# Kernel tuning notes

Measured on AMD Instinct MI355X. Metric: run time of the kernel, lower is better.

The kernel has to match this reference:

```python
import jax, jax.numpy as jnp
import numpy as np

B, S, D, H, HD = 1, 4096, 768, 12, 64
L, C, WIN, NCLS = 2, 256, 256, 64
NC = S // C
V, FF = 50265, 3072
NEG = -1e9
SCALE = np.float32(1.0 / np.sqrt(HD))


def setup_inputs() -> dict:
    key = jax.random.key(0)
    ks = jax.random.split(key, 32)
    p = lambda k, shape: (0.02 * jax.random.normal(k, shape)).astype(jnp.float32)
    inp = {
        'x': jax.random.randint(ks[0], (B, S), 0, V, dtype=jnp.int32),
        'mask_src': jnp.ones((B, S), dtype=jnp.int32),
        'clss': jnp.sort(jax.random.randint(ks[1], (B, NCLS), 0, S, dtype=jnp.int32), axis=-1),
        'segs': jax.random.randint(ks[2], (B, S), 0, 2, dtype=jnp.int32),
        'word_emb': p(ks[3], (V, D)),
        'pos_emb': p(ks[4], (S, D)),
        'type_emb': p(ks[5], (2, D)),
        'ln_e_s': jnp.ones((D,), jnp.float32), 'ln_e_b': jnp.zeros((D,), jnp.float32),
        'Wq': p(ks[6], (L, D, D)), 'bq': jnp.zeros((L, D), jnp.float32),
        'Wk': p(ks[7], (L, D, D)), 'bk': jnp.zeros((L, D), jnp.float32),
        'Wv': p(ks[8], (L, D, D)), 'bv': jnp.zeros((L, D), jnp.float32),
        'Wqg': p(ks[9], (L, D, D)), 'bqg': jnp.zeros((L, D), jnp.float32),
        'Wkg': p(ks[10], (L, D, D)), 'bkg': jnp.zeros((L, D), jnp.float32),
        'Wvg': p(ks[11], (L, D, D)), 'bvg': jnp.zeros((L, D), jnp.float32),
        'Wo': p(ks[12], (L, D, D)), 'bo': jnp.zeros((L, D), jnp.float32),
        'ln1_s': jnp.ones((L, D), jnp.float32), 'ln1_b': jnp.zeros((L, D), jnp.float32),
        'Wf1': p(ks[13], (L, D, FF)), 'bf1': jnp.zeros((L, FF), jnp.float32),
        'Wf2': p(ks[14], (L, FF, D)), 'bf2': jnp.zeros((L, D), jnp.float32),
        'ln2_s': jnp.ones((L, D), jnp.float32), 'ln2_b': jnp.zeros((L, D), jnp.float32),
    }
    return inp


def _layer_norm(x, s, b):
    m = jnp.mean(x, -1, keepdims=True)
    v = jnp.mean((x - m) ** 2, -1, keepdims=True)
    return (x - m) * jax.lax.rsqrt(v + 1e-5) * s + b


def _forward(x, mask_src, clss, segs, word_emb, pos_emb, type_emb, ln_e_s, ln_e_b,
             Wq, bq, Wk, bk, Wv, bv, Wqg, bqg, Wkg, bkg, Wvg, bvg, Wo, bo,
             ln1_s, ln1_b, Wf1, bf1, Wf2, bf2, ln2_s, ln2_b):
    # global positions: union of all clss values, same for every batch row
    g_idx = clss.reshape(-1)                                       # [NCLS]
    is_glb = jnp.zeros((S,), bool).at[g_idx].set(True)             # [S]
    kvalid = (mask_src > 0) & (~is_glb)[None, :]                   # band keys: no pad, no global
    gi = (jnp.arange(NC) * C)[:, None] + jnp.arange(3 * C)[None, :]  # gather idx into padded seq
    rel = jnp.arange(3 * C)[None, :] - (jnp.arange(C)[:, None] + C)  # key offset from query
    band_ok = jnp.abs(rel) <= WIN                                   # [C,3C]
    kv3 = jnp.pad(kvalid, ((0, 0), (C, C)))[:, gi]                  # [B,NC,3C]
    bmask = band_ok[None, None, None, :, :] & kv3[:, None, :, None, :]  # [B,1,NC,C,3C]
    gkey_ok = (mask_src[:, g_idx] > 0)[:, None, None, :]            # [B,1,1,NCLS]
    full_ok = (mask_src > 0)[:, None, None, :]                      # [B,1,1,S]

    h = _layer_norm(word_emb[x] + pos_emb[jnp.arange(S)][None] + type_emb[segs], ln_e_s, ln_e_b)

    for l in range(L):
        q = ((h @ Wq[l] + bq[l]).reshape(B, S, H, HD)) * SCALE
        k = (h @ Wk[l] + bk[l]).reshape(B, S, H, HD)
        v = (h @ Wv[l] + bv[l]).reshape(B, S, H, HD)
        # --- sliding-window band attention ---
        k3 = jnp.pad(k, ((0, 0), (C, C), (0, 0), (0, 0)))[:, gi]    # [B,NC,3C,H,HD]
        v3 = jnp.pad(v, ((0, 0), (C, C), (0, 0), (0, 0)))[:, gi]
        qc = q.reshape(B, NC, C, H, HD)
        sb = jnp.einsum('bnqhd,bnkhd->bhnqk', qc, k3)               # [B,H,NC,C,3C]
        sb = jnp.where(bmask, sb, NEG)
        # --- global keys seen by every query ---
        kg, vg = k[:, g_idx], v[:, g_idx]                           # [B,NCLS,H,HD]
        sg = jnp.einsum('bshd,bkhd->bhsk', q, kg)                   # [B,H,S,NCLS]
        sg = jnp.where(gkey_ok, sg, NEG)
        scores = jnp.concatenate([sg, sb.reshape(B, H, S, 3 * C)], -1)
        probs = jax.nn.softmax(scores, axis=-1)
        pg = probs[..., :NCLS]
        pb = probs[..., NCLS:].reshape(B, H, NC, C, 3 * C)
        out = jnp.einsum('bhnqk,bnkhd->bnqhd', pb, v3).reshape(B, S, H, HD)
        out = out + jnp.einsum('bhsk,bkhd->bshd', pg, vg)
        # --- global query tokens: full attention with *_global projections ---
        hg = h[:, g_idx]                                            # [B,NCLS,D]
        qg = ((hg @ Wqg[l] + bqg[l]).reshape(B, NCLS, H, HD)) * SCALE
        kgf = (h @ Wkg[l] + bkg[l]).reshape(B, S, H, HD)
        vgf = (h @ Wvg[l] + bvg[l]).reshape(B, S, H, HD)
        sfull = jnp.einsum('bqhd,bkhd->bhqk', qg, kgf)              # [B,H,NCLS,S]
        sfull = jnp.where(full_ok, sfull, NEG)
        og = jnp.einsum('bhqk,bkhd->bqhd', jax.nn.softmax(sfull, -1), vgf)
        out = out.at[:, g_idx].set(og)
        # --- output proj, residual, LN, FFN ---
        attn_out = out.reshape(B, S, D) @ Wo[l] + bo[l]
        h = _layer_norm(h + attn_out, ln1_s[l], ln1_b[l])
        ff = jax.nn.gelu(h @ Wf1[l] + bf1[l]) @ Wf2[l] + bf2[l]
        h = _layer_norm(h + ff, ln2_s[l], ln2_b[l])
    return h


def reference(x, mask_src, clss, segs, word_emb, pos_emb, type_emb, ln_e_s, ln_e_b,
              Wq, bq, Wk, bk, Wv, bv, Wqg, bqg, Wkg, bkg, Wvg, bvg, Wo, bo,
              ln1_s, ln1_b, Wf1, bf1, Wf2, bf2, ln2_s, ln2_b):
    return _forward(x, mask_src, clss, segs, word_emb, pos_emb, type_emb, ln_e_s, ln_e_b,
                    Wq, bq, Wk, bk, Wv, bv, Wqg, bqg, Wkg, bkg, Wvg, bvg, Wo, bo,
                    ln1_s, ln1_b, Wf1, bf1, Wf2, bf2, ln2_s, ln2_b)
```

## Files before the change

### kernel.cpp

```cpp
#include <hip/hip_runtime.h>
#include <hip/hip_bf16.h>
#include <cstdint>

#define SEQ  4096
#define DIM  768
#define NH   12
#define HDIM 64
#define NLAYER 2
#define CHK  256
#define WINR 256
#define NCLS 64
#define NCHK 16
#define FFD  3072
#define QSCALE 0.125f
#define LOG2E 1.44269504f
#define QSC2 (QSCALE * LOG2E)
#define SD ((size_t)SEQ * DIM)
#define PS_LD 72
#define TK 64
#define DEFER_THR 8.0f

typedef __attribute__((__vector_size__(16))) float floatx4;
typedef __attribute__((ext_vector_type(8))) __bf16 bf16x8;
typedef __attribute__((ext_vector_type(4))) __bf16 bf16x4;

__device__ __forceinline__ void async16(const void* g, void* l) {
    __builtin_amdgcn_global_load_lds(
        (const __attribute__((address_space(1))) uint32_t*)g,
        (__attribute__((address_space(3))) uint32_t*)l, 16, 0, 0);
}

__device__ __forceinline__ float gelu_f(float x) {
    float x3 = x * x * x;
    return 0.5f * x * (1.0f + tanhf(0.7978845608028654f * (x + 0.044715f * x3)));
}

__global__ __launch_bounds__(256) void embed_ln_kernel(
    const int* __restrict__ x, const int* __restrict__ segs,
    const float* __restrict__ word_emb, const float* __restrict__ pos_emb,
    const float* __restrict__ type_emb, const float* __restrict__ gs,
    const float* __restrict__ gb, float* __restrict__ h, __bf16* __restrict__ hb,
    int* __restrict__ isglb)
{
    int wave = threadIdx.x >> 6, lane = threadIdx.x & 63;
    int s = blockIdx.x * 4 + wave;
    if (lane == 0) isglb[s] = 0;
    int w = x[s], sg = segs[s];
    const float4* wp = (const float4*)(word_emb + (size_t)w * DIM);
    const float4* pp = (const float4*)(pos_emb + (size_t)s * DIM);
    const float4* tp = (const float4*)(type_emb + (size_t)sg * DIM);
    float4 v[3]; float lsum = 0.f;
    #pragma unroll
    for (int i = 0; i < 3; i++) {
        int d4 = lane + i * 64;
        float4 a = wp[d4], b = pp[d4], c = tp[d4];
        float4 r;
        r.x = a.x + b.x + c.x; r.y = a.y + b.y + c.y;
        r.z = a.z + b.z + c.z; r.w = a.w + b.w + c.w;
        v[i] = r; lsum += r.x + r.y + r.z + r.w;
    }
    #pragma unroll
    for (int st = 32; st > 0; st >>= 1) lsum += __shfl_xor(lsum, st);
    float mean = lsum * (1.0f / DIM);
    float lv = 0.f;
    #pragma unroll
    for (int i = 0; i < 3; i++) {
        float dx = v[i].x - mean, dy = v[i].y - mean, dz = v[i].z - mean, dw = v[i].w - mean;
        lv += dx * dx + dy * dy + dz * dz + dw * dw;
    }
    #pragma unroll
    for (int st = 32; st > 0; st >>= 1) lv += __shfl_xor(lv, st);
    float rstd = rsqrtf(lv * (1.0f / DIM) + 1e-5f);
    #pragma unroll
    for (int i = 0; i < 3; i++) {
        int d4 = lane + i * 64;
        float4 s4v = ((const float4*)gs)[d4], b4v = ((const float4*)gb)[d4];
        float4 o;
        o.x = (v[i].x - mean) * rstd * s4v.x + b4v.x;
        o.y = (v[i].y - mean) * rstd * s4v.y + b4v.y;
        o.z = (v[i].z - mean) * rstd * s4v.z + b4v.z;
        o.w = (v[i].w - mean) * rstd * s4v.w + b4v.w;
        ((float4*)(h + (size_t)s * DIM))[d4] = o;
        bf16x4 ob; ob[0] = (__bf16)o.x; ob[1] = (__bf16)o.y;
        ob[2] = (__bf16)o.z; ob[3] = (__bf16)o.w;
        *(bf16x4*)(hb + (size_t)s * DIM + (size_t)d4 * 4) = ob;
    }
}

__global__ __launch_bounds__(256) void add_ln_kernel(
    const float* __restrict__ h, const float* __restrict__ r,
    const float* __restrict__ r2,
    const float* __restrict__ gs, const float* __restrict__ gb,
    float* __restrict__ hout, __bf16* __restrict__ hb)
{
    int wave = threadIdx.x >> 6, lane = threadIdx.x & 63;
    int s = blockIdx.x * 4 + wave;
    const float4* hp = (const float4*)(h + (size_t)s * DIM);
    const float4* rp = (const float4*)(r + (size_t)s * DIM);
    const float4* rp2 = (const float4*)(r2 + (size_t)s * DIM);
    float4 v[3]; float lsum = 0.f;
    #pragma unroll
    for (int i = 0; i < 3; i++) {
        int d4 = lane + i * 64;
        float4 a = hp[d4], b = rp[d4], c = rp2[d4];
        float4 q;
        q.x = a.x + b.x + c.x; q.y = a.y + b.y + c.y;
        q.z = a.z + b.z + c.z; q.w = a.w + b.w + c.w;
        v[i] = q; lsum += q.x + q.y + q.z + q.w;
    }
    #pragma unroll
    for (int st = 32; st > 0; st >>= 1) lsum += __shfl_xor(lsum, st);
    float mean = lsum * (1.0f / DIM);
    float lv = 0.f;
    #pragma unroll
    for (int i = 0; i < 3; i++) {
        float dx = v[i].x - mean, dy = v[i].y - mean, dz = v[i].z - mean, dw = v[i].w - mean;
        lv += dx * dx + dy * dy + dz * dz + dw * dw;
    }
    #pragma unroll
    for (int st = 32; st > 0; st >>= 1) lv += __shfl_xor(lv, st);
    float rstd = rsqrtf(lv * (1.0f / DIM) + 1e-5f);
    #pragma unroll
    for (int i = 0; i < 3; i++) {
        int d4 = lane + i * 64;
        float4 s4v = ((const float4*)gs)[d4], b4v = ((const float4*)gb)[d4];
        float4 o;
        o.x = (v[i].x - mean) * rstd * s4v.x + b4v.x;
        o.y = (v[i].y - mean) * rstd * s4v.y + b4v.y;
        o.z = (v[i].z - mean) * rstd * s4v.z + b4v.z;
        o.w = (v[i].w - mean) * rstd * s4v.w + b4v.w;
        ((float4*)(hout + (size_t)s * DIM))[d4] = o;
        bf16x4 ob; ob[0] = (__bf16)o.x; ob[1] = (__bf16)o.y;
        ob[2] = (__bf16)o.z; ob[3] = (__bf16)o.w;
        *(bf16x4*)(hb + (size_t)s * DIM + (size_t)d4 * 4) = ob;
    }
}

struct TArgs { const float* p14[14]; const float* f1[2]; const float* f2[2]; };
#define DD_ ((size_t)DIM * DIM)
__global__ __launch_bounds__(256) void tpose_setup_kernel(
    TArgs ta, __bf16* __restrict__ Wbf,
    const float* __restrict__ bq, const float* __restrict__ bk,
    const float* __restrict__ bv, const float* __restrict__ bkg,
    const float* __restrict__ bvg, float* __restrict__ bqkv,
    const int* __restrict__ clss, int* __restrict__ isglb)
{
    int b = blockIdx.x;
    if (b >= 17280) {
        int idx = (b - 17280) * 256 + threadIdx.x;
        int l = idx / 3840, c = idx % 3840, j = c / 768, d = c % 768;
        const float* s = (j == 0) ? bq : (j == 1) ? bk : (j == 2) ? bv : (j == 3) ? bkg : bvg;
        bqkv[idx] = s[l * 768 + d];
        if (b == 17280 && threadIdx.x < 64) isglb[clss[threadIdx.x]] = 1;
        return;
    }
    const float* src; __bf16* dst; int K, N, bx, by;
    if (b < 8064) {
        int z = b / 576, rr = b % 576;
        src = ta.p14[z]; dst = Wbf + (size_t)z * DD_;
        K = 768; N = 768; bx = (rr % 24) * 32; by = (rr / 24) * 32;
    } else if (b < 12672) {
        int bb = b - 8064; int z = bb / 2304, rr = bb % 2304;
        src = ta.f1[z]; dst = Wbf + 14 * DD_ + (size_t)z * 4 * DD_;
        K = 768; N = 3072; bx = (rr % 96) * 32; by = (rr / 96) * 32;
    } else {
        int bb = b - 12672; int z = bb / 2304, rr = bb % 2304;
        src = ta.f2[z]; dst = Wbf + 22 * DD_ + (size_t)z * 4 * DD_;
        K = 3072; N = 768; bx = (rr % 24) * 32; by = (rr / 24) * 32;
    }
    __shared__ float tile[32][33];
    int tx = threadIdx.x & 31, ty = threadIdx.x >> 5;
    #pragma unroll
    for (int i = 0; i < 32; i += 8)
        tile[ty + i][tx] = src[(size_t)(by + ty + i) * N + bx + tx];
    __syncthreads();
    #pragma unroll
    for (int i = 0; i < 32; i += 8)
        dst[(size_t)(bx + ty + i) * K + by + tx] = (__bf16)tile[tx][ty + i];
}

template<int TMv, int TNv>
__global__ __launch_bounds__(256) void mfma_gemm_t(
    const __bf16* __restrict__ A, const __bf16* __restrict__ Bt,
    const float* __restrict__ bias, float* __restrict__ Cf,
    float* __restrict__ Cf2, __bf16* __restrict__ Cb,
    int M, int N, int K, float scale, int act)
{
    constexpr int AM = TMv / 32, AN = TNv / 32;
    constexpr int LA = TMv / 32, LB = TNv / 32;
    __shared__ __align__(16) __bf16 As[TMv * TK];
    __shared__ __align__(16) __bf16 Bs[TNv * TK];
    int t = threadIdx.x;
    int wave = t >> 6, lane = t & 63;
    int bm = blockIdx.x * TMv, bn = blockIdx.y * TNv;
    int wm = (wave & 1) * (TMv / 2), wn = (wave >> 1) * (TNv / 2);
    int kz = blockIdx.z;
    int kn = K / (int)gridDim.z, kbeg = kz * kn;
    float* Cfo = (kz == 0) ? Cf : Cf2;

    floatx4 acc[AM][AN];
    #pragma unroll
    for (int i = 0; i < AM; i++)
        #pragma unroll
        for (int j = 0; j < AN; j++) { floatx4 z = {0.f,0.f,0.f,0.f}; acc[i][j] = z; }

    const int mrow = lane & 15, kq = (lane >> 4) * 8;
// ... 174 lines not shown
    int seg = bn / 768;
    int colw_base = bn - seg * 768 + wn;
    float scl = (seg == 0) ? QSC2 : 1.0f;
    unsigned gmask = 0;
    if (seg == 2) {
        #pragma unroll
        for (int mt = 0; mt < 4; mt++)
            #pragma unroll
            for (int rr = 0; rr < 4; rr++)
                gmask |= (unsigned)(is_glb[bm + wm + mt * 16 + row_l + rr] != 0)
                         << (mt * 4 + rr);
    }
    #pragma unroll
    for (int nt = 0; nt < 4; nt++) {
        int col = bn + wn + nt * 16 + col_l;
        int colw = colw_base + nt * 16 + col_l;
        float bs = bias[col];
        #pragma unroll
        for (int mt = 0; mt < 4; mt++) {
            floatx4 v = acc[mt][nt];
            int row0 = bm + wm + mt * 16 + row_l;
            __bf16 t4[4];
            #pragma unroll
            for (int rr = 0; rr < 4; rr++) t4[rr] = (__bf16)((v[rr] + bs) * scl);
            if (seg == 2) {
                #pragma unroll
                for (int rr = 0; rr < 4; rr++)
                    if ((gmask >> (mt * 4 + rr)) & 1)
                        vb[(size_t)(row0 + rr) * 768 + colw] = t4[rr];
            } else if (seg <= 3) {
                __bf16* dst = (seg == 0) ? qb : (seg == 1) ? kb : kgb;
                #pragma unroll
                for (int rr = 0; rr < 4; rr++)
                    dst[(size_t)(row0 + rr) * 768 + colw] = t4[rr];
            }
            if (seg == 2)
                *(uint2*)&vtg[(size_t)colw * SEQ + row0] = *(uint2*)t4;
            if (seg == 4)
                *(uint2*)&vgt[(size_t)colw * SEQ + row0] = *(uint2*)t4;
        }
    }
}

__global__ __launch_bounds__(256) void attn_kernel(
    const __bf16* __restrict__ qb, const __bf16* __restrict__ kb,
    const __bf16* __restrict__ vb, const __bf16* __restrict__ vtg,
    const __bf16* __restrict__ qgbb, const __bf16* __restrict__ kgb,
    const __bf16* __restrict__ vgt,
    const int* __restrict__ clss, const int* __restrict__ mask_src,
    const int* __restrict__ is_glb,
    float* __restrict__ OpartG, float* __restrict__ mlpartG,
    __bf16* __restrict__ outb)
{
    __shared__ __align__(16) __bf16 Kt[4096];
    __shared__ __align__(16) __bf16 Vt[4096];
    __shared__ __align__(16) __bf16 Ps[4][32 * PS_LD];
    __shared__ int kvalid[64];
    __shared__ int gpos[64];

    const int hh = blockIdx.y;
    const int t = threadIdx.x, wave = t >> 6, lane = t & 63;
    const int quad = lane >> 4, col_l = lane & 15, row_l = quad * 4;
    const int l3 = lane & 3, l2h = lane >> 2, l7 = lane & 7, l3h = lane >> 3;
    __bf16* PsW = Ps[wave];

    bf16x8 ones8;
    #pragma unroll
    for (int i = 0; i < 8; i++) ones8[i] = (__bf16)1.0f;

    if (blockIdx.z >= 2) {
        const int sp = blockIdx.x * 2 + (blockIdx.z - 2);
        bf16x8 aq[2];
        {
            const __bf16* qp = qgbb + (size_t)(wave * 16 + col_l) * DIM + hh * HDIM;
            aq[0] = *(const bf16x8*)(qp + quad * 8);
            aq[1] = *(const bf16x8*)(qp + 32 + quad * 8);
        }
        floatx4 oacc[4], oaccE;
        #pragma unroll
        for (int i = 0; i < 4; i++) { floatx4 z = {0.f,0.f,0.f,0.f}; oacc[i] = z; }
        { floatx4 z = {0.f,0.f,0.f,0.f}; oaccE = z; }
        float m4[4];
        #pragma unroll
        for (int r = 0; r < 4; r++) m4[r] = -1e30f;

        for (int tt = 0; tt < 2; tt++) {
            int pos0 = sp * 128 + tt * 64;
            __syncthreads();
            if (t < 64) kvalid[t] = (mask_src[pos0 + t] > 0) ? 1 : 0;
            #pragma unroll
            for (int ii = 0; ii < 2; ii++) {
                int gid = wave * 2 + ii;
                int p = gid >> 2, kbase = (gid & 3) * 16;
                async16(kgb + (size_t)(pos0 + kbase + l2h) * DIM + hh * HDIM + p * 32 + l3 * 8,
                        &Kt[p * 2048 + kbase * 32]);
            }
            #pragma unroll
            for (int ii = 0; ii < 2; ii++) {
                int gid = wave * 2 + ii;
                int p = gid >> 2, dbase = (gid & 3) * 16;
                async16(vgt + (size_t)(hh * HDIM + dbase + l2h) * SEQ + pos0 + p * 32 + l3 * 8,
                        &Vt[p * 2048 + dbase * 32]);
            }
            __builtin_amdgcn_s_waitcnt(0x0f70);
            __syncthreads();

            floatx4 s[4];
            #pragma unroll
            for (int nt = 0; nt < 4; nt++) {
                bf16x8 b0 = *(const bf16x8*)&Kt[(nt * 16 + col_l) * 32 + quad * 8];
                bf16x8 b1 = *(const bf16x8*)&Kt[2048 + (nt * 16 + col_l) * 32 + quad * 8];
                floatx4 z = {0.f,0.f,0.f,0.f};
                z = __builtin_amdgcn_mfma_f32_16x16x32_bf16(aq[0], b0, z, 0,0,0);
                z = __builtin_amdgcn_mfma_f32_16x16x32_bf16(aq[1], b1, z, 0,0,0);
                s[nt] = z;
            }
            #pragma unroll
            for (int nt = 0; nt < 4; nt++) {
                int kvv = kvalid[nt * 16 + col_l];
                #pragma unroll
                for (int rr = 0; rr < 4; rr++)
                    if (!kvv) s[nt][rr] = -1e30f;
            }
            float rmx[4]; int grow = 0;
            #pragma unroll
            for (int rr = 0; rr < 4; rr++) {
                float rm = fmaxf(fmaxf(s[0][rr], s[1][rr]), fmaxf(s[2][rr], s[3][rr]));
                rm = fmaxf(rm, __shfl_xor(rm, 1));
                rm = fmaxf(rm, __shfl_xor(rm, 2));
                rm = fmaxf(rm, __shfl_xor(rm, 4));
                rm = fmaxf(rm, __shfl_xor(rm, 8));
                rmx[rr] = rm;
                grow |= (rm > m4[rr] + DEFER_THR) ? 1 : 0;
            }
            if (__any(grow)) {
                #pragma unroll
                for (int rr = 0; rr < 4; rr++) {
                    float mo = m4[rr];
                    float mn = fmaxf(mo, rmx[rr]);
                    float alpha = exp2f(mo - mn);
                    m4[rr] = mn;
                    #pragma unroll
                    for (int nt = 0; nt < 4; nt++) oacc[nt][rr] *= alpha;
                    oaccE[rr] *= alpha;
                }
            }
            #pragma unroll
            for (int rr = 0; rr < 4; rr++) {
                float mn = m4[rr];
                #pragma unroll
                for (int nt = 0; nt < 4; nt++) {
                    float p = exp2f(s[nt][rr] - mn);
                    PsW[(row_l + rr) * PS_LD + nt * 16 + col_l] = (__bf16)p;
                }
            }
            bf16x8 ap0 = *(const bf16x8*)&PsW[col_l * PS_LD + quad * 8];
            bf16x8 ap1 = *(const bf16x8*)&PsW[col_l * PS_LD + 32 + quad * 8];
            oaccE = __builtin_amdgcn_mfma_f32_16x16x32_bf16(ap0, ones8, oaccE, 0,0,0);
            oaccE = __builtin_amdgcn_mfma_f32_16x16x32_bf16(ap1, ones8, oaccE, 0,0,0);
            #pragma unroll
            for (int nt = 0; nt < 4; nt++) {
                bf16x8 b0 = *(const bf16x8*)&Vt[(nt * 16 + col_l) * 32 + quad * 8];
                bf16x8 b1 = *(const bf16x8*)&Vt[2048 + (nt * 16 + col_l) * 32 + quad * 8];
                oacc[nt] = __builtin_amdgcn_mfma_f32_16x16x32_bf16(ap0, b0, oacc[nt], 0,0,0);
                oacc[nt] = __builtin_amdgcn_mfma_f32_16x16x32_bf16(ap1, b1, oacc[nt], 0,0,0);
            }
        }
        size_t base = (size_t)(hh * 32 + sp) * 64;
        #pragma unroll
        for (int nt = 0; nt < 4; nt++)
            #pragma unroll
            for (int rr = 0; rr < 4; rr++)
                OpartG[(base + wave * 16 + row_l + rr) * 64 + nt * 16 + col_l] = oacc[nt][rr];
        if (col_l == 0) {
            #pragma unroll
            for (int rr = 0; rr < 4; rr++) {
                mlpartG[(base + wave * 16 + row_l + rr) * 2]     = m4[rr];
                mlpartG[(base + wave * 16 + row_l + rr) * 2 + 1] = oaccE[rr];
            }
        }
        return;
    }

    const int n = blockIdx.x, qh = blockIdx.z;
    const int qw = qh * 128 + wave * 32;

    if (t < 64) gpos[t] = clss[t];

    bf16x8 aq[2][2];
    #pragma unroll
    for (int mt = 0; mt < 2; mt++) {
        const __bf16* qp = qb + (size_t)(n * CHK + qw + mt * 16 + col_l) * DIM + hh * HDIM;
        aq[mt][0] = *(const bf16x8*)(qp + quad * 8);
        aq[mt][1] = *(const bf16x8*)(qp + 32 + quad * 8);
    }

    floatx4 oacc[2][4];
    floatx4 oaccE[2];
    #pragma unroll
    for (int i = 0; i < 2; i++) {
        #pragma unroll
        for (int j = 0; j < 4; j++) { floatx4 z = {0.f,0.f,0.f,0.f}; oacc[i][j] = z; }
        floatx4 z = {0.f,0.f,0.f,0.f}; oaccE[i] = z;
    }
    float mrw[8];
    #pragma unroll
    for (int r = 0; r < 8; r++) mrw[r] = -1e30f;

    for (int tt = 0; tt < 11; tt++) {
        __syncthreads();
        int jbase = -1;
        int isglob = (tt == 0);
        if (isglob) {
            if (t < 64) kvalid[t] = (mask_src[gpos[t]] > 0) ? 1 : 0;
            #pragma unroll
            for (int g = 0; g < 2; g++) {
                int gid = wave * 2 + g;
                int p = gid >> 2, kbase = (gid & 3) * 16;
                int pos = gpos[kbase + l2h];
                async16(kb + (size_t)pos * DIM + hh * HDIM + p * 32 + l3 * 8,
                        &Kt[p * 2048 + kbase * 32]);
            }
            __bf16* Vrow = &Ps[0][0];
            #pragma unroll
            for (int g = 0; g < 2; g++) {
                int cg = wave * 2 + g;
                int pos = gpos[cg * 8 + l3h];
                async16(vb + (size_t)pos * DIM + hh * HDIM + l7 * 8,
                        &Vrow[cg * 64 * 8]);
            }
        } else {
            int jt = qh * 2 + tt - 1;
            jbase = jt * 64;
            if (t < 64) {
                int pos = n * CHK + jbase + t - CHK;
                kvalid[t] = (pos >= 0 && pos < SEQ && mask_src[pos] > 0
                             && is_glb[pos] == 0) ? 1 : 0;
            }
            int s0 = n * CHK + jbase - CHK;
            #pragma unroll
            for (int g = 0; g < 2; g++) {
                int gid = wave * 2 + g;
                int p = gid >> 2, kbase = (gid & 3) * 16;
                int pos = s0 + kbase + l2h; pos = min(max(pos, 0), SEQ - 1);
                async16(kb + (size_t)pos * DIM + hh * HDIM + p * 32 + l3 * 8,
                        &Kt[p * 2048 + kbase * 32]);
            }
            #pragma unroll
            for (int g = 0; g < 2; g++) {
                int gid = wave * 2 + g;
                int p = gid >> 2, dbase = (gid & 3) * 16;
                int d = dbase + l2h;
                int s = s0 + p * 32 + l3 * 8; s = min(max(s, 0), SEQ - 8);
                async16(vtg + (size_t)(hh * HDIM + d) * SEQ + s,
                        &Vt[p * 2048 + dbase * 32]);
            }
        }
        __builtin_amdgcn_s_waitcnt(0x0f70);
        __syncthreads();
        if (isglob) {
            const __bf16* Vrow = &Ps[0][0];
            for (int idx = t; idx < 4096; idx += 256) {
                int key = idx >> 6, d = idx & 63;
                Vt[(key >> 5) * 2048 + d * 32 + (key & 31)] = Vrow[idx];
            }
            __syncthreads();
        } else {
            if (jbase + 63 < qw || jbase > qw + 543) continue;
        }

        bf16x8 bkf[4][2];
        #pragma unroll
        for (int nt = 0; nt < 4; nt++) {
            bkf[nt][0] = *(const bf16x8*)&Kt[(nt * 16 + col_l) * 32 + quad * 8];
            bkf[nt][1] = *(const bf16x8*)&Kt[2048 + (nt * 16 + col_l) * 32 + quad * 8];
        }
        int kv[4];
        #pragma unroll
        for (int nt = 0; nt < 4; nt++) kv[nt] = kvalid[nt * 16 + col_l];

        #pragma unroll
        for (int mt = 0; mt < 2; mt++) {
            floatx4 s[4];
            #pragma unroll
            for (int nt = 0; nt < 4; nt++) {
                floatx4 z = {0.f,0.f,0.f,0.f};
                z = __builtin_amdgcn_mfma_f32_16x16x32_bf16(aq[mt][0], bkf[nt][0], z, 0,0,0);
                z = __builtin_amdgcn_mfma_f32_16x16x32_bf16(aq[mt][1], bkf[nt][1], z, 0,0,0);
                s[nt] = z;
            }
            #pragma unroll
            for (int nt = 0; nt < 4; nt++)
                #pragma unroll
                for (int rr = 0; rr < 4; rr++) {
                    int ok = kv[nt];
                    if (!isglob) {
                        int i = qw + mt * 16 + row_l + rr;
                        int rel = jbase + nt * 16 + col_l - i;
                        ok = ok && (rel >= 0) && (rel <= 2 * WINR);
                    }
                    if (!ok) s[nt][rr] = -1e30f;
                }
            float rmx[4]; int grow = 0;
            #pragma unroll
            for (int rr = 0; rr < 4; rr++) {
                float rm = fmaxf(fmaxf(s[0][rr], s[1][rr]), fmaxf(s[2][rr], s[3][rr]));
                rm = fmaxf(rm, __shfl_xor(rm, 1));
                rm = fmaxf(rm, __shfl_xor(rm, 2));
                rm = fmaxf(rm, __shfl_xor(rm, 4));
                rm = fmaxf(rm, __shfl_xor(rm, 8));
                rmx[rr] = rm;
                grow |= (rm > mrw[mt * 4 + rr] + DEFER_THR) ? 1 : 0;
            }
            if (__any(grow)) {
                #pragma unroll
                for (int rr = 0; rr < 4; rr++) {
                    int ri = mt * 4 + rr;
                    float mo = mrw[ri];
                    float mn = fmaxf(mo, rmx[rr]);
                    float alpha = exp2f(mo - mn);
                    mrw[ri] = mn;
                    #pragma unroll
                    for (int nt = 0; nt < 4; nt++) oacc[mt][nt][rr] *= alpha;
                    oaccE[mt][rr] *= alpha;
                }
            }
            #pragma unroll
            for (int rr = 0; rr < 4; rr++) {
                float mn = mrw[mt * 4 + rr];
                #pragma unroll
                for (int nt = 0; nt < 4; nt++) {
                    float p = exp2f(s[nt][rr] - mn);
                    PsW[(mt * 16 + row_l + rr) * PS_LD + nt * 16 + col_l] = (__bf16)p;
                }
            }
        }
        bf16x8 bvf[4][2], ap[2][2];
        #pragma unroll
        for (int nt = 0; nt < 4; nt++) {
            bvf[nt][0] = *(const bf16x8*)&Vt[(nt * 16 + col_l) * 32 + quad * 8];
            bvf[nt][1] = *(const bf16x8*)&Vt[2048 + (nt * 16 + col_l) * 32 + quad * 8];
        }
        #pragma unroll
        for (int mt = 0; mt < 2; mt++) {
            ap[mt][0] = *(const bf16x8*)&PsW[(mt * 16 + col_l) * PS_LD + quad * 8];
            ap[mt][1] = *(const bf16x8*)&PsW[(mt * 16 + col_l) * PS_LD + 32 + quad * 8];
        }
        #pragma unroll
        for (int mt = 0; mt < 2; mt++) {
            oaccE[mt] = __builtin_amdgcn_mfma_f32_16x16x32_bf16(ap[mt][0], ones8, oaccE[mt], 0,0,0);
            oaccE[mt] = __builtin_amdgcn_mfma_f32_16x16x32_bf16(ap[mt][1], ones8, oaccE[mt], 0,0,0);
            #pragma unroll
            for (int nt = 0; nt < 4; nt++) {
                oacc[mt][nt] = __builtin_amdgcn_mfma_f32_16x16x32_bf16(
                    ap[mt][0], bvf[nt][0], oacc[mt][nt], 0,0,0);
                oacc[mt][nt] = __builtin_amdgcn_mfma_f32_16x16x32_bf16(
                    ap[mt][1], bvf[nt][1], oacc[mt][nt], 0,0,0);
            }
        }
    }

    #pragma unroll
    for (int mt = 0; mt < 2; mt++) {
        #pragma unroll
        for (int rr = 0; rr < 4; rr++) {
            int srow = n * CHK + qw + mt * 16 + row_l + rr;
            if (is_glb[srow]) continue;
            float inv = 1.0f / oaccE[mt][rr];
            #pragma unroll
            for (int nt = 0; nt < 4; nt++)
                outb[(size_t)srow * DIM + hh * HDIM + nt * 16 + col_l] =
                    (__bf16)(oacc[mt][nt][rr] * inv);
        }
    }
}

__global__ __launch_bounds__(64) void gq_finalize(
    const float* __restrict__ OpartG, const float* __restrict__ mlpartG,
    const int* __restrict__ clss, __bf16* __restrict__ outb)
{
    int r = blockIdx.x, hh = blockIdx.y, d = threadIdx.x;
    float M = -1e30f;
    for (int sp = 0; sp < 32; sp++)
        M = fmaxf(M, mlpartG[(((size_t)hh * 32 + sp) * 64 + r) * 2]);
    float L = 0.f, acc = 0.f;
    for (int sp = 0; sp < 32; sp++) {
        size_t b = ((size_t)hh * 32 + sp) * 64 + r;
        float w = exp2f(mlpartG[b * 2] - M);
        L += mlpartG[b * 2 + 1] * w;
        acc += w * OpartG[b * 64 + d];
    }
    int pos = clss[r];
    outb[(size_t)pos * DIM + hh * HDIM + d] = (__bf16)(acc / L);
}

extern "C" void kernel_launch(void* const* d_in, const int* in_sizes, int n_in,
                              void* d_out, int out_size, void* d_ws, size_t ws_size,
                              hipStream_t stream)
{
    const int* x        = (const int*)d_in[0];
    const int* mask_src = (const int*)d_in[1];
    const int* clss     = (const int*)d_in[2];
    const int* segs     = (const int*)d_in[3];
    const float* word_emb = (const float*)d_in[4];
    const float* pos_emb  = (const float*)d_in[5];
    const float* type_emb = (const float*)d_in[6];
    const float* ln_e_s   = (const float*)d_in[7];
    const float* ln_e_b   = (const float*)d_in[8];
    const float* Wq  = (const float*)d_in[9];
    const float* bq  = (const float*)d_in[10];
    const float* Wk  = (const float*)d_in[11];
    const float* bk  = (const float*)d_in[12];
    const float* Wv  = (const float*)d_in[13];
    const float* bv  = (const float*)d_in[14];
    const float* Wqg = (const float*)d_in[15];
    const float* bqg = (const float*)d_in[16];
    const float* Wkg = (const float*)d_in[17];
    const float* bkg = (const float*)d_in[18];
    const float* Wvg = (const float*)d_in[19];
    const float* bvg = (const float*)d_in[20];
    const float* Wo  = (const float*)d_in[21];
    const float* bo  = (const float*)d_in[22];
    const float* ln1_s = (const float*)d_in[23];
    const float* ln1_b = (const float*)d_in[24];
    const float* Wf1 = (const float*)d_in[25];
    const float* bf1 = (const float*)d_in[26];
    const float* Wf2 = (const float*)d_in[27];
    const float* bf2 = (const float*)d_in[28];
    const float* ln2_s = (const float*)d_in[29];
    const float* ln2_b = (const float*)d_in[30];

    const size_t DD = (size_t)DIM * DIM;
    float* ws = (float*)d_ws;
    float*  h    = ws;
    float*  s4   = ws + SD;
    __bf16* hb   = (__bf16*)(ws + 2 * SD);
    __bf16* b6b  = (__bf16*)(ws + 2 * SD) + SD;
    __bf16* qb   = (__bf16*)(ws + 3 * SD);
    __bf16* kb   = (__bf16*)(ws + 3 * SD) + SD;
    __bf16* vb   = (__bf16*)(ws + 4 * SD);
    __bf16* vtg  = (__bf16*)(ws + 4 * SD) + SD;
    __bf16* kgb  = (__bf16*)(ws + 5 * SD);
    __bf16* vgt  = (__bf16*)(ws + 5 * SD) + SD;
    __bf16* gelu_b = qb;
    float* extra = ws + 6 * SD;
    __bf16* Wbf   = (__bf16*)extra;
    float* after_w = extra + 15 * DD;
    float* bqkv   = after_w;
    float* OpartG = bqkv + 7680;
    float* mlpartG= OpartG + 1572864;
    float* s4b    = mlpartG + 49152;
    __bf16* qgbb  = (__bf16*)(s4b + SD);
    int*   isglb  = (int*)(qgbb + (size_t)NCLS * DIM);

    embed_ln_kernel<<<SEQ / 4, 256, 0, stream>>>(x, segs, word_emb, pos_emb, type_emb,
                                                 ln_e_s, ln_e_b, h, hb, isglb);
    {
        TArgs ta{};
        ta.p14[0] = Wq;        ta.p14[1] = Wk;        ta.p14[2] = Wv;
        ta.p14[3] = Wkg;       ta.p14[4] = Wvg;
        ta.p14[5] = Wq + DD;   ta.p14[6] = Wk + DD;   ta.p14[7] = Wv + DD;
        ta.p14[8] = Wkg + DD;  ta.p14[9] = Wvg + DD;
        ta.p14[10] = Wo;       ta.p14[11] = Wo + DD;
        ta.p14[12] = Wqg;      ta.p14[13] = Wqg + DD;
        ta.f1[0] = Wf1; ta.f1[1] = Wf1 + (size_t)DIM * FFD;
        ta.f2[0] = Wf2; ta.f2[1] = Wf2 + (size_t)FFD * DIM;
        tpose_setup_kernel<<<17310, 256, 0, stream>>>(ta, Wbf, bq, bk, bv, bkg, bvg,
                                                      bqkv, clss, isglb);
    }

    for (int l = 0; l < NLAYER; l++) {
        const float* bqg_l = bqg + (size_t)l * DIM;
        const float* bo_l  = bo  + (size_t)l * DIM;
        const float* bf1_l = bf1 + (size_t)l * FFD;
        const float* bf2_l = bf2 + (size_t)l * DIM;

        mfma_gemm_proj<<<dim3(SEQ / 128, 36), 256, 0, stream>>>(
            hb, Wbf + (size_t)l * 5 * DD, bqkv + l * 3840,
            qb, kb, vb, vtg, kgb, vgt, DIM,
            Wbf + 12 * DD + (size_t)l * DD, bqg_l, clss, qgbb, isglb);
        attn_kernel<<<dim3(NCHK, NH, 4), 256, 0, stream>>>(
            qb, kb, vb, vtg, qgbb, kgb, vgt, clss, mask_src, isglb,
            OpartG, mlpartG, b6b);
        gq_finalize<<<dim3(NCLS, NH), 64, 0, stream>>>(OpartG, mlpartG, clss, b6b);
        mfma_gemm_t<128, 64><<<dim3(SEQ / 128, DIM / 64, 2), 256, 0, stream>>>(
            b6b, Wbf + 10 * DD + (size_t)l * DD, bo_l, s4, s4b, nullptr,
            SEQ, DIM, DIM, 1.0f, 0);
        add_ln_kernel<<<SEQ / 4, 256, 0, stream>>>(h, s4, s4b, ln1_s + (size_t)l * DIM,
                                                   ln1_b + (size_t)l * DIM, h, hb);
        mfma_gemm_t<128, 128><<<dim3(SEQ / 128, FFD / 128, 1), 256, 0, stream>>>(
            hb, Wbf + 14 * DD + (size_t)l * 4 * DD, bf1_l, nullptr, nullptr, gelu_b,
            SEQ, FFD, DIM, 1.0f, 1);
        mfma_gemm_t<128, 64><<<dim3(SEQ / 128, DIM / 64, 2), 256, 0, stream>>>(
            gelu_b, Wbf + 22 * DD + (size_t)l * 4 * DD, bf2_l, s4, s4b, nullptr,
            SEQ, DIM, FFD, 1.0f, 0);
        add_ln_kernel<<<SEQ / 4, 256, 0, stream>>>(h, s4, s4b, ln2_s + (size_t)l * DIM,
                                                   ln2_b + (size_t)l * DIM,
                                                   (l == NLAYER - 1) ? (float*)d_out : h, hb);
    }
}
```

Baseline: 702.1 us.

## Double-buffer attention K/V tiles and fold embedding LN into setup kernel

Measured after the change: 714.5 us. No clear change (+1.8%).

```diff
diff --git a/kernel.cpp b/kernel.cpp
--- a/kernel.cpp
+++ b/kernel.cpp
@@ -16,7 +16,7 @@
 #define LOG2E 1.44269504f
 #define QSC2 (QSCALE * LOG2E)
 #define SD ((size_t)SEQ * DIM)
-#define PS_LD 72
+#define PS_LD 68
 #define TK 64
 #define DEFER_THR 8.0f
 
@@ -33,58 +33,6 @@
 __device__ __forceinline__ float gelu_f(float x) {
     float x3 = x * x * x;
     return 0.5f * x * (1.0f + tanhf(0.7978845608028654f * (x + 0.044715f * x3)));
-}
-
-__global__ __launch_bounds__(256) void embed_ln_kernel(
-    const int* __restrict__ x, const int* __restrict__ segs,
-    const float* __restrict__ word_emb, const float* __restrict__ pos_emb,
-    const float* __restrict__ type_emb, const float* __restrict__ gs,
-    const float* __restrict__ gb, float* __restrict__ h, __bf16* __restrict__ hb,
-    int* __restrict__ isglb)
-{
-    int wave = threadIdx.x >> 6, lane = threadIdx.x & 63;
-    int s = blockIdx.x * 4 + wave;
-    if (lane == 0) isglb[s] = 0;
-    int w = x[s], sg = segs[s];
-    const float4* wp = (const float4*)(word_emb + (size_t)w * DIM);
-    const float4* pp = (const float4*)(pos_emb + (size_t)s * DIM);
-    const float4* tp = (const float4*)(type_emb + (size_t)sg * DIM);
-    float4 v[3]; float lsum = 0.f;
-    #pragma unroll
-    for (int i = 0; i < 3; i++) {
-        int d4 = lane + i * 64;
-        float4 a = wp[d4], b = pp[d4], c = tp[d4];
-        float4 r;
-        r.x = a.x + b.x + c.x; r.y = a.y + b.y + c.y;
-        r.z = a.z + b.z + c.z; r.w = a.w + b.w + c.w;
-        v[i] = r; lsum += r.x + r.y + r.z + r.w;
-    }
-    #pragma unroll
-    for (int st = 32; st > 0; st >>= 1) lsum += __shfl_xor(lsum, st);
-    float mean = lsum * (1.0f / DIM);
-    float lv = 0.f;
-    #pragma unroll
-    for (int i = 0; i < 3; i++) {
-        float dx = v[i].x - mean, dy = v[i].y - mean, dz = v[i].z - mean, dw = v[i].w - mean;
-        lv += dx * dx + dy * dy + dz * dz + dw * dw;
-    }
-    #pragma unroll
-    for (int st = 32; st > 0; st >>= 1) lv += __shfl_xor(lv, st);
-    float rstd = rsqrtf(lv * (1.0f / DIM) + 1e-5f);
-    #pragma unroll
-    for (int i = 0; i < 3; i++) {
-        int d4 = lane + i * 64;
-        float4 s4v = ((const float4*)gs)[d4], b4v = ((const float4*)gb)[d4];
-        float4 o;
-        o.x = (v[i].x - mean) * rstd * s4v.x + b4v.x;
-        o.y = (v[i].y - mean) * rstd * s4v.y + b4v.y;
-        o.z = (v[i].z - mean) * rstd * s4v.z + b4v.z;
-        o.w = (v[i].w - mean) * rstd * s4v.w + b4v.w;
-        ((float4*)(h + (size_t)s * DIM))[d4] = o;
-        bf16x4 ob; ob[0] = (__bf16)o.x; ob[1] = (__bf16)o.y;
-        ob[2] = (__bf16)o.z; ob[3] = (__bf16)o.w;
-        *(bf16x4*)(hb + (size_t)s * DIM + (size_t)d4 * 4) = ob;
-    }
 }
 
 __global__ __launch_bounds__(256) void add_ln_kernel(
@@ -136,22 +84,74 @@
     }
 }
 
-struct TArgs { const float* p14[14]; const float* f1[2]; const float* f2[2]; };
+struct TArgs {
+    const float* p14[14]; const float* f1[2]; const float* f2[2];
+    const int* x; const int* segs;
+    const float* word_emb; const float* pos_emb; const float* type_emb;
+    const float* ln_e_s; const float* ln_e_b;
+};
 #define DD_ ((size_t)DIM * DIM)
 __global__ __launch_bounds__(256) void tpose_setup_kernel(
     TArgs ta, __bf16* __restrict__ Wbf,
     const float* __restrict__ bq, const float* __restrict__ bk,
     const float* __restrict__ bv, const float* __restrict__ bkg,
     const float* __restrict__ bvg, float* __restrict__ bqkv,
-    const int* __restrict__ clss, int* __restrict__ isglb)
+    const int* __restrict__ clss, int* __restrict__ isglb,
+    float* __restrict__ h, __bf16* __restrict__ hb)
 {
     int b = blockIdx.x;
+    if (b >= 17310) {
+        int wave = threadIdx.x >> 6, lane = threadIdx.x & 63;
+        int s = (b - 17310) * 4 + wave;
+        unsigned long long mb = __ballot(clss[lane] == s);
+        if (lane == 0) isglb[s] = (mb != 0ull) ? 1 : 0;
+        int w = ta.x[s], sg = ta.segs[s];
+        const float4* wp = (const float4*)(ta.word_emb + (size_t)w * DIM);
+        const float4* pp = (const float4*)(ta.pos_emb + (size_t)s * DIM);
+        const float4* tp = (const float4*)(ta.type_emb + (size_t)sg * DIM);
+        float4 v[3]; float lsum = 0.f;
+        #pragma unroll
+        for (int i = 0; i < 3; i++) {
+            int d4 = lane + i * 64;
+            float4 a = wp[d4], bb = pp[d4], c = tp[d4];
+            float4 r;
+            r.x = a.x + bb.x + c.x; r.y = a.y + bb.y + c.y;
+            r.z = a.z + bb.z + c.z; r.w = a.w + bb.w + c.w;
+            v[i] = r; lsum += r.x + r.y + r.z + r.w;
+        }
+        #pragma unroll
+        for (int st = 32; st > 0; st >>= 1) lsum += __shfl_xor(lsum, st);
+        float mean = lsum * (1.0f / DIM);
+        float lv = 0.f;
+        #pragma unroll
+        for (int i = 0; i < 3; i++) {
+            float dx = v[i].x - mean, dy = v[i].y - mean, dz = v[i].z - mean, dw = v[i].w - mean;
+            lv += dx * dx + dy * dy + dz * dz + dw * dw;
+        }
+        #pragma unroll
+        for (int st = 32; st > 0; st >>= 1) lv += __shfl_xor(lv, st);
+        float rstd = rsqrtf(lv * (1.0f / DIM) + 1e-5f);
+        #pragma unroll
+        for (int i = 0; i < 3; i++) {
+            int d4 = lane + i * 64;
+            float4 s4v = ((const float4*)ta.ln_e_s)[d4], b4v = ((const float4*)ta.ln_e_b)[d4];
+            float4 o;
+            o.x = (v[i].x - mean) * rstd * s4v.x + b4v.x;
+            o.y = (v[i].y - mean) * rstd * s4v.y + b4v.y;
+            o.z = (v[i].z - mean) * rstd * s4v.z + b4v.z;
+            o.w = (v[i].w - mean) * rstd * s4v.w + b4v.w;
+            ((float4*)(h + (size_t)s * DIM))[d4] = o;
+            bf16x4 ob; ob[0] = (__bf16)o.x; ob[1] = (__bf16)o.y;
+            ob[2] = (__bf16)o.z; ob[3] = (__bf16)o.w;
+            *(bf16x4*)(hb + (size_t)s * DIM + (size_t)d4 * 4) = ob;
+        }
+        return;
+    }
     if (b >= 17280) {
         int idx = (b - 17280) * 256 + threadIdx.x;
         int l = idx / 3840, c = idx % 3840, j = c / 768, d = c % 768;
         const float* s = (j == 0) ? bq : (j == 1) ? bk : (j == 2) ? bv : (j == 3) ? bkg : bvg;
         bqkv[idx] = s[l * 768 + d];
-        if (b == 17280 && threadIdx.x < 64) isglb[clss[threadIdx.x]] = 1;
         return;
     }
     const float* src; __bf16* dst; int K, N, bx, by;
@@ -432,10 +432,10 @@
     float* __restrict__ OpartG, float* __restrict__ mlpartG,
     __bf16* __restrict__ outb)
 {
-    __shared__ __align__(16) __bf16 Kt[4096];
-    __shared__ __align__(16) __bf16 Vt[4096];
+    __shared__ __align__(16) __bf16 Kt[2][4096];
+    __shared__ __align__(16) __bf16 Vt[2][4096];
     __shared__ __align__(16) __bf16 Ps[4][32 * PS_LD];
-    __shared__ int kvalid[64];
+    __shared__ int kvalid[2][64];
     __shared__ int gpos[64];
 
     const int hh = blockIdx.y;
@@ -464,32 +464,35 @@
         #pragma unroll
         for (int r = 0; r < 4; r++) m4[r] = -1e30f;
 
-        for (int tt = 0; tt < 2; tt++) {
+        auto stage_gq = [&](int tt, int buf) {
             int pos0 = sp * 128 + tt * 64;
-            __syncthreads();
-            if (t < 64) kvalid[t] = (mask_src[pos0 + t] > 0) ? 1 : 0;
+            if (t < 64) kvalid[buf][t] = (mask_src[pos0 + t] > 0) ? 1 : 0;
             #pragma unroll
             for (int ii = 0; ii < 2; ii++) {
                 int gid = wave * 2 + ii;
                 int p = gid >> 2, kbase = (gid & 3) * 16;
                 async16(kgb + (size_t)(pos0 + kbase + l2h) * DIM + hh * HDIM + p * 32 + l3 * 8,
-                        &Kt[p * 2048 + kbase * 32]);
-            }
-            #pragma unroll
-            for (int ii = 0; ii < 2; ii++) {
-                int gid = wave * 2 + ii;
-                int p = gid >> 2, dbase = (gid & 3) * 16;
+                        &Kt[buf][p * 2048 + kbase * 32]);
+                int dbase = (gid & 3) * 16;
                 async16(vgt + (size_t)(hh * HDIM + dbase + l2h) * SEQ + pos0 + p * 32 + l3 * 8,
-                        &Vt[p * 2048 + dbase * 32]);
-            }
-            __builtin_amdgcn_s_waitcnt(0x0f70);
-            __syncthreads();
+                        &Vt[buf][p * 2048 + dbase * 32]);
+            }
+        };
+
+        stage_gq(0, 0);
+        __builtin_amdgcn_s_waitcnt(0x0f70);
+        __syncthreads();
+
+        for (int tt = 0; tt < 2; tt++) {
+            if (tt == 0) stage_gq(1, 1);
+            const __bf16* KtB = Kt[tt];
+            const __bf16* VtB = Vt[tt];
 
             floatx4 s[4];
             #pragma unroll
             for (int nt = 0; nt < 4; nt++) {
-                bf16x8 b0 = *(const bf16x8*)&Kt[(nt * 16 + col_l) * 32 + quad * 8];
-                bf16x8 b1 = *(const bf16x8*)&Kt[2048 + (nt * 16 + col_l) * 32 + quad * 8];
+                bf16x8 b0 = *(const bf16x8*)&KtB[(nt * 16 + col_l) * 32 + quad * 8];
+                bf16x8 b1 = *(const bf16x8*)&KtB[2048 + (nt * 16 + col_l) * 32 + quad * 8];
                 floatx4 z = {0.f,0.f,0.f,0.f};
                 z = __builtin_amdgcn_mfma_f32_16x16x32_bf16(aq[0], b0, z, 0,0,0);
                 z = __builtin_amdgcn_mfma_f32_16x16x32_bf16(aq[1], b1, z, 0,0,0);
@@ -497,7 +500,7 @@
             }
             #pragma unroll
             for (int nt = 0; nt < 4; nt++) {
-                int kvv = kvalid[nt * 16 + col_l];
+                int kvv = kvalid[tt][nt * 16 + col_l];
                 #pragma unroll
                 for (int rr = 0; rr < 4; rr++)
                     if (!kvv) s[nt][rr] = -1e30f;
@@ -540,10 +543,14 @@
             oaccE = __builtin_amdgcn_mfma_f32_16x16x32_bf16(ap1, ones8, oaccE, 0,0,0);
             #pragma unroll
             for (int nt = 0; nt < 4; nt++) {
-                bf16x8 b0 = *(const bf16x8*)&Vt[(nt * 16 + col_l) * 32 + quad * 8];
-                bf16x8 b1 = *(const bf16x8*)&Vt[2048 + (nt * 16 + col_l) * 32 + quad * 8];
+                bf16x8 b0 = *(const bf16x8*)&VtB[(nt * 16 + col_l) * 32 + quad * 8];
+                bf16x8 b1 = *(const bf16x8*)&VtB[2048 + (nt * 16 + col_l) * 32 + quad * 8];
                 oacc[nt] = __builtin_amdgcn_mfma_f32_16x16x32_bf16(ap0, b0, oacc[nt], 0,0,0);
                 oacc[nt] = __builtin_amdgcn_mfma_f32_16x16x32_bf16(ap1, b1, oacc[nt], 0,0,0);
+            }
+            if (tt == 0) {
+                __builtin_amdgcn_s_waitcnt(0x0f70);
+                __syncthreads();
             }
         }
         size_t base = (size_t)(hh * 32 + sp) * 64;
@@ -566,6 +573,7 @@
     const int qw = qh * 128 + wave * 32;
 
     if (t < 64) gpos[t] = clss[t];
+    __syncthreads();
 
     bf16x8 aq[2][2];
     #pragma unroll
@@ -587,157 +595,155 @@
     #pragma unroll
     for (int r = 0; r < 8; r++) mrw[r] = -1e30f;
 
-    for (int tt = 0; tt < 11; tt++) {
-        __syncthreads();
-        int jbase = -1;
+    __bf16* PsStage = &Ps[0][0];
+
+    auto stage_band = [&](int tt , int buf) {
+        int jbase = (qh * 2 + tt - 1) * 64;
+        int s0 = n * CHK + jbase - CHK;
+        if (t < 64) {
+            int pos = s0 + t;
+            kvalid[buf][t] = (pos >= 0 && pos < SEQ && mask_src[pos] > 0
+                              && is_glb[pos] == 0) ? 1 : 0;
+        }
+        #pragma unroll
+        for (int g = 0; g < 2; g++) {
+            int gid = wave * 2 + g;
+            int p = gid >> 2, kbase = (gid & 3) * 16;
+            int pos = s0 + kbase + l2h; pos = min(max(pos, 0), SEQ - 1);
+            async16(kb + (size_t)pos * DIM + hh * HDIM + p * 32 + l3 * 8,
+                    &Kt[buf][p * 2048 + kbase * 32]);
+            int dbase = (gid & 3) * 16;
+            int d = dbase + l2h;
+            int s = s0 + p * 32 + l3 * 8; s = min(max(s, 0), SEQ - 8);
+            async16(vtg + (size_t)(hh * HDIM + d) * SEQ + s,
+                    &Vt[buf][p * 2048 + dbase * 32]);
+        }
+    };
+
+    {
+        if (t < 64) kvalid[0][t] = (mask_src[gpos[t]] > 0) ? 1 : 0;
+        #pragma unroll
+        for (int g = 0; g < 2; g++) {
+            int gid = wave * 2 + g;
+            int p = gid >> 2, kbase = (gid & 3) * 16;
+            int pos = gpos[kbase + l2h];
+            async16(kb + (size_t)pos * DIM + hh * HDIM + p * 32 + l3 * 8,
+                    &Kt[0][p * 2048 + kbase * 32]);
+            int cg = wave * 2 + g;
+            int pos2 = gpos[cg * 8 + l3h];
+            async16(vb + (size_t)pos2 * DIM + hh * HDIM + l7 * 8,
+                    &PsStage[cg * 512]);
+        }
+    }
+    __builtin_amdgcn_s_waitcnt(0x0f70);
+    __syncthreads();
+    for (int idx = t; idx < 4096; idx += 256) {
+        int key = idx >> 6, d = idx & 63;
+        Vt[0][(key >> 5) * 2048 + d * 32 + (key & 31)] = PsStage[idx];
+    }
+    __syncthreads();
+
+    for (int tt = 0; tt <= 10; tt++) {
+        if (tt < 10) stage_band(tt + 1, (tt + 1) & 1);
+        int buf = tt & 1;
         int isglob = (tt == 0);
-        if (isglob) {
-            if (t < 64) kvalid[t] = (mask_src[gpos[t]] > 0) ? 1 : 0;
-            #pragma unroll
-            for (int g = 0; g < 2; g++) {
-                int gid = wave * 2 + g;
-                int p = gid >> 2, kbase = (gid & 3) * 16;
-                int pos = gpos[kbase + l2h];
-                async16(kb + (size_t)pos * DIM + hh * HDIM + p * 32 + l3 * 8,
-                        &Kt[p * 2048 + kbase * 32]);
-            }
-            __bf16* Vrow = &Ps[0][0];
-            #pragma unroll
-            for (int g = 0; g < 2; g++) {
-                int cg = wave * 2 + g;
-                int pos = gpos[cg * 8 + l3h];
-                async16(vb + (size_t)pos * DIM + hh * HDIM + l7 * 8,
-                        &Vrow[cg * 64 * 8]);
-            }
-        } else {
-            int jt = qh * 2 + tt - 1;
-            jbase = jt * 64;
-            if (t < 64) {
-                int pos = n * CHK + jbase + t - CHK;
-                kvalid[t] = (pos >= 0 && pos < SEQ && mask_src[pos] > 0
-                             && is_glb[pos] == 0) ? 1 : 0;
-            }
-            int s0 = n * CHK + jbase - CHK;
-            #pragma unroll
-            for (int g = 0; g < 2; g++) {
-                int gid = wave * 2 + g;
-                int p = gid >> 2, kbase = (gid & 3) * 16;
-                int pos = s0 + kbase + l2h; pos = min(max(pos, 0), SEQ - 1);
-                async16(kb + (size_t)pos * DIM + hh * HDIM + p * 32 + l3 * 8,
-                        &Kt[p * 2048 + kbase * 32]);
-            }
-            #pragma unroll
-            for (int g = 0; g < 2; g++) {
-                int gid = wave * 2 + g;
-                int p = gid >> 2, dbase = (gid & 3) * 16;
-                int d = dbase + l2h;
-                int s = s0 + p * 32 + l3 * 8; s = min(max(s, 0), SEQ - 8);
-                async16(vtg + (size_t)(hh * HDIM + d) * SEQ + s,
-                        &Vt[p * 2048 + dbase * 32]);
+        int jbase = isglob ? -1 : (qh * 2 + tt - 1) * 64;
+        bool doit = isglob || !(jbase + 63 < qw || jbase > qw + 543);
+        if (doit) {
+            const __bf16* KtB = Kt[buf];
+            const __bf16* VtB = Vt[buf];
+            bf16x8 bkf[4][2];
+            #pragma unroll
+            for (int nt = 0; nt < 4; nt++) {
+                bkf[nt][0] = *(const bf16x8*)&KtB[(nt * 16 + col_l) * 32 + quad * 8];
+                bkf[nt][1] = *(const bf16x8*)&KtB[2048 + (nt * 16 + col_l) * 32 + quad * 8];
+            }
+            int kv[4];
+            #pragma unroll
+            for (int nt = 0; nt < 4; nt++) kv[nt] = kvalid[buf][nt * 16 + col_l];
+
+            #pragma unroll
+            for (int mt = 0; mt < 2; mt++) {
+                floatx4 s[4];
+                #pragma unroll
+                for (int nt = 0; nt < 4; nt++) {
+                    floatx4 z = {0.f,0.f,0.f,0.f};
+                    z = __builtin_amdgcn_mfma_f32_16x16x32_bf16(aq[mt][0], bkf[nt][0], z, 0,0,0);
+                    z = __builtin_amdgcn_mfma_f32_16x16x32_bf16(aq[mt][1], bkf[nt][1], z, 0,0,0);
+                    s[nt] = z;
+                }
+                #pragma unroll
+                for (int nt = 0; nt < 4; nt++)
+                    #pragma unroll
+                    for (int rr = 0; rr < 4; rr++) {
+                        int ok = kv[nt];
+                        if (!isglob) {
+                            int i = qw + mt * 16 + row_l + rr;
+                            int rel = jbase + nt * 16 + col_l - i;
+                            ok = ok && (rel >= 0) && (rel <= 2 * WINR);
+                        }
+                        if (!ok) s[nt][rr] = -1e30f;
+                    }
+                float rmx[4]; int grow = 0;
+                #pragma unroll
+                for (int rr = 0; rr < 4; rr++) {
+                    float rm = fmaxf(fmaxf(s[0][rr], s[1][rr]), fmaxf(s[2][rr], s[3][rr]));
+                    rm = fmaxf(rm, __shfl_xor(rm, 1));
+                    rm = fmaxf(rm, __shfl_xor(rm, 2));
+                    rm = fmaxf(rm, __shfl_xor(rm, 4));
+                    rm = fmaxf(rm, __shfl_xor(rm, 8));
+                    rmx[rr] = rm;
+                    grow |= (rm > mrw[mt * 4 + rr] + DEFER_THR) ? 1 : 0;
+                }
+                if (__any(grow)) {
+                    #pragma unroll
+                    for (int rr = 0; rr < 4; rr++) {
+                        int ri = mt * 4 + rr;
+                        float mo = mrw[ri];
+                        float mn = fmaxf(mo, rmx[rr]);
+                        float alpha = exp2f(mo - mn);
+                        mrw[ri] = mn;
+                        #pragma unroll
+                        for (int nt = 0; nt < 4; nt++) oacc[mt][nt][rr] *= alpha;
+                        oaccE[mt][rr] *= alpha;
+                    }
+                }
+                #pragma unroll
+                for (int rr = 0; rr < 4; rr++) {
+                    float mn = mrw[mt * 4 + rr];
+                    #pragma unroll
+                    for (int nt = 0; nt < 4; nt++) {
+                        float p = exp2f(s[nt][rr] - mn);
+                        PsW[(mt * 16 + row_l + rr) * PS_LD + nt * 16 + col_l] = (__bf16)p;
+                    }
+                }
+            }
+            bf16x8 bvf[4][2], ap[2][2];
+            #pragma unroll
+            for (int nt = 0; nt < 4; nt++) {
+                bvf[nt][0] = *(const bf16x8*)&VtB[(nt * 16 + col_l) * 32 + quad * 8];
+                bvf[nt][1] = *(const bf16x8*)&VtB[2048 + (nt * 16 + col_l) * 32 + quad * 8];
+            }
+            #pragma unroll
+            for (int mt = 0; mt < 2; mt++) {
+                ap[mt][0] = *(const bf16x8*)&PsW[(mt * 16 + col_l) * PS_LD + quad * 8];
+                ap[mt][1] = *(const bf16x8*)&PsW[(mt * 16 + col_l) * PS_LD + 32 + quad * 8];
+            }
+            #pragma unroll
+            for (int mt = 0; mt < 2; mt++) {
+                oaccE[mt] = __builtin_amdgcn_mfma_f32_16x16x32_bf16(ap[mt][0], ones8, oaccE[mt], 0,0,0);
+                oaccE[mt] = __builtin_amdgcn_mfma_f32_16x16x32_bf16(ap[mt][1], ones8, oaccE[mt], 0,0,0);
+                #pragma unroll
+                for (int nt = 0; nt < 4; nt++) {
+                    oacc[mt][nt] = __builtin_amdgcn_mfma_f32_16x16x32_bf16(
+                        ap[mt][0], bvf[nt][0], oacc[mt][nt], 0,0,0);
+                    oacc[mt][nt] = __builtin_amdgcn_mfma_f32_16x16x32_bf16(
+                        ap[mt][1], bvf[nt][1], oacc[mt][nt], 0,0,0);
+                }
             }
         }
         __builtin_amdgcn_s_waitcnt(0x0f70);
         __syncthreads();
-        if (isglob) {
-            const __bf16* Vrow = &Ps[0][0];
-            for (int idx = t; idx < 4096; idx += 256) {
-                int key = idx >> 6, d = idx & 63;
-                Vt[(key >> 5) * 2048 + d * 32 + (key & 31)] = Vrow[idx];
-            }
-            __syncthreads();
-        } else {
-            if (jbase + 63 < qw || jbase > qw + 543) continue;
-        }
-
-        bf16x8 bkf[4][2];
-        #pragma unroll
-        for (int nt = 0; nt < 4; nt++) {
-            bkf[nt][0] = *(const bf16x8*)&Kt[(nt * 16 + col_l) * 32 + quad * 8];
-            bkf[nt][1] = *(const bf16x8*)&Kt[2048 + (nt * 16 + col_l) * 32 + quad * 8];
-        }
-        int kv[4];
-        #pragma unroll
-        for (int nt = 0; nt < 4; nt++) kv[nt] = kvalid[nt * 16 + col_l];
-
-        #pragma unroll
-        for (int mt = 0; mt < 2; mt++) {
-            floatx4 s[4];
-            #pragma unroll
-            for (int nt = 0; nt < 4; nt++) {
-                floatx4 z = {0.f,0.f,0.f,0.f};
-                z = __builtin_amdgcn_mfma_f32_16x16x32_bf16(aq[mt][0], bkf[nt][0], z, 0,0,0);
-                z = __builtin_amdgcn_mfma_f32_16x16x32_bf16(aq[mt][1], bkf[nt][1], z, 0,0,0);
-                s[nt] = z;
-            }
-            #pragma unroll
-            for (int nt = 0; nt < 4; nt++)
-                #pragma unroll
-                for (int rr = 0; rr < 4; rr++) {
-                    int ok = kv[nt];
-                    if (!isglob) {
-                        int i = qw + mt * 16 + row_l + rr;
-                        int rel = jbase + nt * 16 + col_l - i;
-                        ok = ok && (rel >= 0) && (rel <= 2 * WINR);
-                    }
-                    if (!ok) s[nt][rr] = -1e30f;
-                }
-            float rmx[4]; int grow = 0;
-            #pragma unroll
-            for (int rr = 0; rr < 4; rr++) {
-                float rm = fmaxf(fmaxf(s[0][rr], s[1][rr]), fmaxf(s[2][rr], s[3][rr]));
-                rm = fmaxf(rm, __shfl_xor(rm, 1));
-                rm = fmaxf(rm, __shfl_xor(rm, 2));
-                rm = fmaxf(rm, __shfl_xor(rm, 4));
-                rm = fmaxf(rm, __shfl_xor(rm, 8));
-                rmx[rr] = rm;
-                grow |= (rm > mrw[mt * 4 + rr] + DEFER_THR) ? 1 : 0;
-            }
-            if (__any(grow)) {
-                #pragma unroll
-                for (int rr = 0; rr < 4; rr++) {
-                    int ri = mt * 4 + rr;
-                    float mo = mrw[ri];
-                    float mn = fmaxf(mo, rmx[rr]);
-                    float alpha = exp2f(mo - mn);
-                    mrw[ri] = mn;
-                    #pragma unroll
-                    for (int nt = 0; nt < 4; nt++) oacc[mt][nt][rr] *= alpha;
-                    oaccE[mt][rr] *= alpha;
-                }
-            }
-            #pragma unroll
-            for (int rr = 0; rr < 4; rr++) {
-                float mn = mrw[mt * 4 + rr];
-                #pragma unroll
-                for (int nt = 0; nt < 4; nt++) {
-                    float p = exp2f(s[nt][rr] - mn);
-                    PsW[(mt * 16 + row_l + rr) * PS_LD + nt * 16 + col_l] = (__bf16)p;
-                }
-            }
-        }
-        bf16x8 bvf[4][2], ap[2][2];
-        #pragma unroll
-        for (int nt = 0; nt < 4; nt++) {
-            bvf[nt][0] = *(const bf16x8*)&Vt[(nt * 16 + col_l) * 32 + quad * 8];
-            bvf[nt][1] = *(const bf16x8*)&Vt[2048 + (nt * 16 + col_l) * 32 + quad * 8];
-        }
-        #pragma unroll
-        for (int mt = 0; mt < 2; mt++) {
-            ap[mt][0] = *(const bf16x8*)&PsW[(mt * 16 + col_l) * PS_LD + quad * 8];
-            ap[mt][1] = *(const bf16x8*)&PsW[(mt * 16 + col_l) * PS_LD + 32 + quad * 8];
-        }
-        #pragma unroll
-        for (int mt = 0; mt < 2; mt++) {
-            oaccE[mt] = __builtin_amdgcn_mfma_f32_16x16x32_bf16(ap[mt][0], ones8, oaccE[mt], 0,0,0);
-            oaccE[mt] = __builtin_amdgcn_mfma_f32_16x16x32_bf16(ap[mt][1], ones8, oaccE[mt], 0,0,0);
-            #pragma unroll
-            for (int nt = 0; nt < 4; nt++) {
-                oacc[mt][nt] = __builtin_amdgcn_mfma_f32_16x16x32_bf16(
-                    ap[mt][0], bvf[nt][0], oacc[mt][nt], 0,0,0);
-                oacc[mt][nt] = __builtin_amdgcn_mfma_f32_16x16x32_bf16(
-                    ap[mt][1], bvf[nt][1], oacc[mt][nt], 0,0,0);
-            }
-        }
     }
 
     #pragma unroll
@@ -833,8 +839,6 @@
     __bf16* qgbb  = (__bf16*)(s4b + SD);
     int*   isglb  = (int*)(qgbb + (size_t)NCLS * DIM);
 
-    embed_ln_kernel<<<SEQ / 4, 256, 0, stream>>>(x, segs, word_emb, pos_emb, type_emb,
-                                                 ln_e_s, ln_e_b, h, hb, isglb);
     {
         TArgs ta{};
         ta.p14[0] = Wq;        ta.p14[1] = Wk;        ta.p14[2] = Wv;
@@ -845,8 +849,11 @@
         ta.p14[12] = Wqg;      ta.p14[13] = Wqg + DD;
         ta.f1[0] = Wf1; ta.f1[1] = Wf1 + (size_t)DIM * FFD;
         ta.f2[0] = Wf2; ta.f2[1] = Wf2 + (size_t)FFD * DIM;
-        tpose_setup_kernel<<<17310, 256, 0, stream>>>(ta, Wbf, bq, bk, bv, bkg, bvg,
-                                                      bqkv, clss, isglb);
+        ta.x = x; ta.segs = segs;
+        ta.word_emb = word_emb; ta.pos_emb = pos_emb; ta.type_emb = type_emb;
+        ta.ln_e_s = ln_e_s; ta.ln_e_b = ln_e_b;
+        tpose_setup_kernel<<<18334, 256, 0, stream>>>(ta, Wbf, bq, bk, bv, bkg, bvg,
+                                                      bqkv, clss, isglb, h, hb);
     }
 
     for (int l = 0; l < NLAYER; l++) {
```
